# Kernel tuning notes

Measured on AMD Instinct MI355X. Metric: run time of the kernel, lower is better.

The kernel has to match this reference:

```python
import jax, jax.numpy as jnp
import numpy as np

D_MODEL, N_HEADS, D_C, D_FF, N_EXPERTS, TOP_K = 1024, 16, 128, 2048, 8, 2
HEAD_DIM = D_MODEL // N_HEADS
THETA = 10000.0
RMS_EPS = float(np.finfo(np.float32).eps)  # torch nn.RMSNorm default eps


def rmsnorm(x, w):
    var = jnp.mean(x * x, axis=-1, keepdims=True)
    return x * jax.lax.rsqrt(var + RMS_EPS) * w


def rotate_half(x):
    x1, x2 = jnp.split(x, 2, axis=-1)
    return jnp.concatenate([-x2, x1], axis=-1)


def rope_cos_sin(ts):
    # ts: (B, L) float timestamps -> cos, sin: (B, L, HEAD_DIM)
    freqs = 1.0 / THETA ** (jnp.arange(0, HEAD_DIM, 2, dtype=jnp.float32) / HEAD_DIM)
    t = ts[..., None] * freqs            # (B, L, HEAD_DIM//2)
    emb = jnp.concatenate([t, t], axis=-1)
    return jnp.cos(emb), jnp.sin(emb)


def setup_inputs() -> dict:
    key = jax.random.key(0)
    ks = jax.random.split(key, 16)
    B, L, D = 4, 1024, D_MODEL
    s = 0.02
    inp = {
        "x": jax.random.normal(ks[0], (B, L, D), jnp.float32),
        "timestamps_q": jnp.tile(jnp.arange(L, dtype=jnp.float32), (B, 1)),
        "timestamps_kv": jnp.tile(jnp.arange(L, dtype=jnp.float32), (B, 1)),
        "attn_norm_w": jnp.ones((D,), jnp.float32),
        "ffn_norm_w": jnp.ones((D,), jnp.float32),
        "w_kv_c": jax.random.normal(ks[1], (D_C, D), jnp.float32) * s,
        "w_kc_up": jax.random.normal(ks[2], (D, D_C), jnp.float32) * s,
        "w_vc_up": jax.random.normal(ks[3], (D, D_C), jnp.float32) * s,
        "w_qr": jax.random.normal(ks[4], (D, D), jnp.float32) * s,
        "w_kr": jax.random.normal(ks[5], (D, D), jnp.float32) * s,
        "w_o": jax.random.normal(ks[6], (D, D), jnp.float32) * s,
        "gate_w": jax.random.normal(ks[7], (N_EXPERTS, D), jnp.float32) * s,
        "expert_bias": jnp.zeros((N_EXPERTS,), jnp.float32),
        "w1": jax.random.normal(ks[8], (N_EXPERTS, 2 * D_FF, D), jnp.float32) * s,
        "w2": jax.random.normal(ks[9], (N_EXPERTS, D, 2 * D_FF), jnp.float32) * s,
    }
    return inp


def reference(x, timestamps_q, timestamps_kv, attn_norm_w, ffn_norm_w,
              w_kv_c, w_kc_up, w_vc_up, w_qr, w_kr, w_o,
              gate_w, expert_bias, w1, w2):
    B, L, D = x.shape
    H, hd = N_HEADS, HEAD_DIM
    scale = hd ** -0.5

    # ---- MLA attention (pre-norm) ----
    h = rmsnorm(x, attn_norm_w)
    c_kv = h @ w_kv_c.T                                    # (B,L,d_c)
    k_c = (c_kv @ w_kc_up.T).reshape(B, L, H, hd).transpose(0, 2, 1, 3)
    v_c = (c_kv @ w_vc_up.T).reshape(B, L, H, hd).transpose(0, 2, 1, 3)
    q_r = (h @ w_qr.T).reshape(B, L, H, hd).transpose(0, 2, 1, 3)
    k_r = (h @ w_kr.T).reshape(B, L, H, hd).transpose(0, 2, 1, 3)

    cos_q, _sin_q = rope_cos_sin(timestamps_q)
    cos_k, _sin_k = rope_cos_sin(timestamps_kv)
    cos_q = cos_q[:, None]  # (B,1,L,hd)
    cos_k = cos_k[:, None]
    # Faithful to source: apply_rotary_pos_emb(q, k, cos_q, cos_k) -> sin := cos_k
    q_r = q_r * cos_q + rotate_half(q_r) * cos_k
    k_r = k_r * cos_q + rotate_half(k_r) * cos_k

    qs = q_r * scale
    attn = jnp.einsum("bhqd,bhkd->bhqk", qs, k_c) + jnp.einsum("bhqd,bhkd->bhqk", qs, k_r)
    attn_w = jax.nn.softmax(attn, axis=-1)
    out = jnp.einsum("bhqk,bhkd->bhqd", attn_w, v_c)
    out = out.transpose(0, 2, 1, 3).reshape(B, L, D) @ w_o.T
    x1 = x + out

    # ---- MoE FFN (pre-norm) ----
    hn = rmsnorm(x1, ffn_norm_w).reshape(-1, D)            # (T, D)
    T = hn.shape[0]
    gate_logits = hn @ gate_w.T + expert_bias              # (T, E)
    gate_probs = jax.nn.softmax(gate_logits, axis=-1)
    topk_w, topk_i = jax.lax.top_k(gate_probs, TOP_K)
    topk_w = topk_w / jnp.sum(topk_w, axis=-1, keepdims=True)

    # dense (T, E) routing weights (top-k indices are unique per token)
    wd = jnp.zeros((T, N_EXPERTS), x.dtype).at[jnp.arange(T)[:, None], topk_i].add(topk_w)

    hmid = jax.nn.silu(jnp.einsum("td,ekd->tek", hn, w1))  # (T,E,2*d_ff)
    y = jnp.einsum("tek,edk->ted", hmid, w2)               # (T,E,D)
    moe_out = jnp.einsum("ted,te->td", y, wd).reshape(B, L, D)

    expert_counts = jnp.zeros((N_EXPERTS,), jnp.float32).at[topk_i.ravel()].add(1.0)
    return x1 + moe_out, expert_counts
```

## Files before the change

kernel.cpp:

```cpp
#include <hip/hip_runtime.h>
#include <hip/hip_bf16.h>

typedef __hip_bfloat16 bf16;
typedef __attribute__((ext_vector_type(8))) unsigned short ushort8v;
typedef __bf16 bf16x8 __attribute__((ext_vector_type(8)));
typedef float f32x4 __attribute__((ext_vector_type(4)));

#define NTOK 4096
#define DMODEL 1024
#define NHEADS 16
#define HD 64
#define DC 128
#define DFF2 4096
#define NEXP 8
#define LSEQ 1024
#define NBATCH 4
#define RMS_EPS 1.1920928955078125e-07f

union U8 { ushort8v u; bf16x8 b; };

__device__ __forceinline__ float bf2f(unsigned short u) {
  return __uint_as_float(((unsigned int)u) << 16);
}
__device__ __forceinline__ unsigned short f2bf(float f) {
  unsigned int u = __float_as_uint(f);
  unsigned int r = (u + 0x7FFF + ((u >> 16) & 1)) >> 16;
  return (unsigned short)r;
}
__device__ __forceinline__ void gload_lds16(const unsigned short* g, unsigned short* l) {
  __builtin_amdgcn_global_load_lds(
      (__attribute__((address_space(1))) void*)(const_cast<unsigned short*>(g)),
      (__attribute__((address_space(3))) void*)(l), 16, 0, 0);
}

__global__ __launch_bounds__(256)
void rmsnorm_kernel(const float* __restrict__ x, const float* __restrict__ w,
                    float* __restrict__ o, unsigned short* __restrict__ ob) {
  int t = blockIdx.x;
  int tid = threadIdx.x;
  const float4* xr = (const float4*)(x + (size_t)t * DMODEL);
  float4 v = xr[tid];
  float ss = v.x * v.x + v.y * v.y + v.z * v.z + v.w * v.w;
#pragma unroll
  for (int off = 32; off > 0; off >>= 1) ss += __shfl_xor(ss, off);
  __shared__ float red[4];
  int wid = tid >> 6, lane = tid & 63;
  if (lane == 0) red[wid] = ss;
  __syncthreads();
  float tot = red[0] + red[1] + red[2] + red[3];
  float scale = rsqrtf(tot * (1.0f / DMODEL) + RMS_EPS);
  float4 wv = ((const float4*)w)[tid];
  float4 ov;
  ov.x = v.x * scale * wv.x;
  ov.y = v.y * scale * wv.y;
  ov.z = v.z * scale * wv.z;
  ov.w = v.w * scale * wv.w;
  if (o) ((float4*)(o + (size_t)t * DMODEL))[tid] = ov;
  if (ob) {
    unsigned short* orow = ob + (size_t)t * DMODEL + tid * 4;
    orow[0] = f2bf(ov.x); orow[1] = f2bf(ov.y);
    orow[2] = f2bf(ov.z); orow[3] = f2bf(ov.w);
  }
}

__global__ __launch_bounds__(256)
void cvt_bf16_kernel(const float* __restrict__ in, unsigned short* __restrict__ o, int n8) {
  int stride = gridDim.x * 256;
  for (int i = blockIdx.x * 256 + threadIdx.x; i < n8; i += stride) {
    float4 a = ((const float4*)in)[2 * i];
    float4 b = ((const float4*)in)[2 * i + 1];
    ushort8v u;
    u[0] = f2bf(a.x); u[1] = f2bf(a.y); u[2] = f2bf(a.z); u[3] = f2bf(a.w);
    u[4] = f2bf(b.x); u[5] = f2bf(b.y); u[6] = f2bf(b.z); u[7] = f2bf(b.w);
    *(ushort8v*)(o + (size_t)i * 8) = u;
  }
}

__global__ __launch_bounds__(256)
void gemm_bf16(const unsigned short* __restrict__ Ab, const unsigned short* __restrict__ Wb,
               float* __restrict__ Cf, const float* __restrict__ addend, int N, int K) {
  __shared__ __align__(16) unsigned short As[128 * 64];
  __shared__ __align__(16) unsigned short Bs[128 * 64];
  int row0 = blockIdx.y * 128;
  int col0 = blockIdx.x * 128;
  int tid = threadIdx.x;
  int w = tid >> 6, l = tid & 63;
  int lr = l >> 3;
  int lc = (l & 7) * 8;

  const unsigned short* aSrc[4];
  const unsigned short* bSrc[4];
#pragma unroll
  for (int i = 0; i < 4; ++i) {
    aSrc[i] = Ab + (size_t)(row0 + i * 32 + w * 8 + lr) * K + lc;
    bSrc[i] = Wb + (size_t)(col0 + i * 32 + w * 8 + lr) * K + lc;
  }

  f32x4 acc[4][4] = {};
  int wr = w >> 1, wc = w & 1;
  int ln = l & 15, lq = l >> 4;

  for (int k0 = 0; k0 < K; k0 += 64) {
#pragma unroll
    for (int i = 0; i < 4; ++i) {
      gload_lds16(aSrc[i] + k0, &As[(i * 4 + w) * 512]);
      gload_lds16(bSrc[i] + k0, &Bs[(i * 4 + w) * 512]);
    }
    __syncthreads();
#pragma unroll
    for (int kk = 0; kk < 2; ++kk) {
      bf16x8 af[4], bfr[4];
#pragma unroll
      for (int m = 0; m < 4; ++m)
        af[m] = *(const bf16x8*)&As[(wr * 64 + m * 16 + ln) * 64 + kk * 32 + lq * 8];
#pragma unroll
      for (int n = 0; n < 4; ++n)
        bfr[n] = *(const bf16x8*)&Bs[(wc * 64 + n * 16 + ln) * 64 + kk * 32 + lq * 8];
#pragma unroll
      for (int m = 0; m < 4; ++m)
#pragma unroll
        for (int n = 0; n < 4; ++n)
          acc[m][n] = __builtin_amdgcn_mfma_f32_16x16x32_bf16(af[m], bfr[n], acc[m][n], 0, 0, 0);
    }
    __syncthreads();
  }

#pragma unroll
  for (int m = 0; m < 4; ++m) {
#pragma unroll
    for (int j = 0; j < 4; ++j) {
      int row = row0 + wr * 64 + m * 16 + lq * 4 + j;
      float* crow = Cf + (size_t)row * N + col0 + wc * 64 + ln;
      const float* arow = addend ? addend + (size_t)row * N + col0 + wc * 64 + ln : nullptr;
#pragma unroll
      for (int n = 0; n < 4; ++n) {
        float vv = acc[m][n][j];
        if (addend) vv += arow[n * 16];
        crow[n * 16] = vv;
      }
    }
  }
}

__global__ __launch_bounds__(256)
void gemm_proj(const unsigned short* __restrict__ Ab, const unsigned short* __restrict__ Wcat,
               float* __restrict__ d0, float* __restrict__ d1, float* __restrict__ d2,
               int c1, int c2, int s0, int s1, int s2, int K) {
  __shared__ __align__(16) unsigned short As[128 * 64];
  __shared__ __align__(16) unsigned short Bs[128 * 64];
  int row0 = blockIdx.y * 128;
  int col0 = blockIdx.x * 128;
  int tid = threadIdx.x;
  int w = tid >> 6, l = tid & 63;
  int lr = l >> 3;
  int lc = (l & 7) * 8;

  const unsigned short* aSrc[4];
  const unsigned short* bSrc[4];
#pragma unroll
  for (int i = 0; i < 4; ++i) {
    aSrc[i] = Ab + (size_t)(row0 + i * 32 + w * 8 + lr) * K + lc;
    bSrc[i] = Wcat + (size_t)(col0 + i * 32 + w * 8 + lr) * K + lc;
  }

  f32x4 acc[4][4] = {};
  int wr = w >> 1, wc = w & 1;
  int ln = l & 15, lq = l >> 4;

  for (int k0 = 0; k0 < K; k0 += 64) {
#pragma unroll
    for (int i = 0; i < 4; ++i) {
      gload_lds16(aSrc[i] + k0, &As[(i * 4 + w) * 512]);
      gload_lds16(bSrc[i] + k0, &Bs[(i * 4 + w) * 512]);
    }
    __syncthreads();
#pragma unroll
    for (int kk = 0; kk < 2; ++kk) {
      bf16x8 af[4], bfr[4];
#pragma unroll
      for (int m = 0; m < 4; ++m)
        af[m] = *(const bf16x8*)&As[(wr * 64 + m * 16 + ln) * 64 + kk * 32 + lq * 8];
#pragma unroll
      for (int n = 0; n < 4; ++n)
        bfr[n] = *(const bf16x8*)&Bs[(wc * 64 + n * 16 + ln) * 64 + kk * 32 + lq * 8];
#pragma unroll
      for (int m = 0; m < 4; ++m)
#pragma unroll
        for (int n = 0; n < 4; ++n)
          acc[m][n] = __builtin_amdgcn_mfma_f32_16x16x32_bf16(af[m], bfr[n], acc[m][n], 0, 0, 0);
    }
    __syncthreads();
  }

  float* dst;
  int cb, stride;
  if (col0 < c1) { dst = d0; cb = 0; stride = s0; }
  else if (col0 < c2) { dst = d1; cb = c1; stride = s1; }
  else { dst = d2; cb = c2; stride = s2; }
#pragma unroll
  for (int m = 0; m < 4; ++m) {
#pragma unroll
    for (int j = 0; j < 4; ++j) {
      int row = row0 + wr * 64 + m * 16 + lq * 4 + j;
      float* crow = dst + (size_t)row * stride + (col0 - cb) + wc * 64 + ln;
#pragma unroll
      for (int n = 0; n < 4; ++n) crow[n * 16] = acc[m][n][j];
    }
  }
}

template <int MODE>
__global__ __launch_bounds__(512, 2)
void moe_gemm256(const unsigned short* __restrict__ A, const unsigned short* __restrict__ W_,
                 unsigned short* __restrict__ Cb, const int* __restrict__ tok2e,
                 const int* __restrict__ ebase, const int* __restrict__ icnt) {
  constexpr int N = (MODE == 0) ? DFF2 : DMODEL;
  constexpr int K = (MODE == 0) ? DMODEL : DFF2;
  __shared__ __align__(16) unsigned short As[2][256 * 64];
  __shared__ __align__(16) unsigned short Bs[2][256 * 64];
  int e = blockIdx.z;
  int base = ebase[e];
  int cnt = icnt[e];
  int row0 = blockIdx.y * 256;
  if (row0 >= cnt) return;
  int col0 = blockIdx.x * 256;
  int tid = threadIdx.x;
  int w = tid >> 6, l = tid & 63;
  int lr = l >> 3, lc = (l & 7) * 8;

  const unsigned short* aP[4];
  const unsigned short* bP[4];
#pragma unroll
  for (int p = 0; p < 4; ++p) {
    int r = row0 + p * 64 + w * 8 + lr;
    r = r < cnt ? r : cnt - 1;
    if (MODE == 0)
      aP[p] = A + (size_t)(tok2e[base + r] >> 1) * K + lc;
    else
      aP[p] = A + (size_t)(base + r) * K + lc;
    bP[p] = W_ + (size_t)e * N * K + (size_t)(col0 + p * 64 + w * 8 + lr) * K + lc;
  }

  f32x4 acc[8][4] = {};
  int wm = w >> 2, wn = w & 3;
  int ln = l & 15, lq = l >> 4;

  constexpr int NT = K / 64;
#pragma unroll
  for (int p = 0; p < 4; ++p) {
    gload_lds16(aP[p], &As[0][(p * 64 + w * 8) * 64]);
    gload_lds16(bP[p], &Bs[0][(p * 64 + w * 8) * 64]);
  }
  __syncthreads();
  int cur = 0;
  for (int t = 0; t < NT; ++t) {
    if (t + 1 < NT) {
      int k0 = (t + 1) * 64;
#pragma unroll
      for (int p = 0; p < 4; ++p) {
        gload_lds16(aP[p] + k0, &As[cur ^ 1][(p * 64 + w * 8) * 64]);
        gload_lds16(bP[p] + k0, &Bs[cur ^ 1][(p * 64 + w * 8) * 64]);
      }
    }
    {
      const unsigned short* ab = &As[cur][0];
      const unsigned short* bb = &Bs[cur][0];
#pragma unroll
      for (int kk = 0; kk < 2; ++kk) {
        bf16x8 af[8], bfr[4];
#pragma unroll
        for (int m = 0; m < 8; ++m)
          af[m] = *(const bf16x8*)&ab[(wm * 128 + m * 16 + ln) * 64 + kk * 32 + lq * 8];
#pragma unroll
        for (int n = 0; n < 4; ++n)
          bfr[n] = *(const bf16x8*)&bb[(wn * 64 + n * 16 + ln) * 64 + kk * 32 + lq * 8];
#pragma unroll
        for (int m = 0; m < 8; ++m)
#pragma unroll
          for (int n = 0; n < 4; ++n)
            acc[m][n] = __builtin_amdgcn_mfma_f32_16x16x32_bf16(af[m], bfr[n], acc[m][n], 0, 0, 0);
      }
    }
    __syncthreads();
    cur ^= 1;
  }

#pragma unroll
  for (int m = 0; m < 8; ++m) {
#pragma unroll
    for (int j = 0; j < 4; ++j) {
      int r = row0 + wm * 128 + m * 16 + lq * 4 + j;
      if (r < cnt) {
        if (MODE == 0) {
          unsigned short* orow = Cb + (size_t)(base + r) * N + col0 + wn * 64 + ln;
#pragma unroll
          for (int n = 0; n < 4; ++n) {
            float v = acc[m][n][j];
            orow[n * 16] = f2bf(v / (1.f + __expf(-v)));
          }
        } else {
          int t2 = tok2e[base + r];
          unsigned short* orow = Cb + (size_t)t2 * N + col0 + wn * 64 + ln;
#pragma unroll
          for (int n = 0; n < 4; ++n) orow[n * 16] = f2bf(acc[m][n][j]);
        }
      }
    }
  }
}

__global__ __launch_bounds__(256)
void rope_kernel(float* __restrict__ q, float* __restrict__ k,
                 const float* __restrict__ kc, const float* __restrict__ tsq,
                 const float* __restrict__ tskv) {
  int t = blockIdx.x;
  int tid = threadIdx.x;
  __shared__ float cq[32], ck[32];
  if (tid < 32) {
    float fr = __expf(-(float)(2 * tid) * (1.0f / HD) * 9.210340371976184f);
    cq[tid] = cosf(tsq[t] * fr);
    ck[tid] = cosf(tskv[t] * fr);
  }
  __syncthreads();
  size_t rb = (size_t)t * DMODEL;
  for (int p = tid; p < 512; p += 256) {
    int hh = p >> 5, d = p & 31;
    int c1 = hh * 64 + d, c2 = c1 + 32;
    float cqd = cq[d], ckd = ck[d];
    float q1 = q[rb + c1], q2 = q[rb + c2];
    q[rb + c1] = (q1 * cqd - q2 * ckd) * 0.125f;
    q[rb + c2] = (q2 * cqd + q1 * ckd) * 0.125f;
    float k1 = k[rb + c1], k2 = k[rb + c2];
    k[rb + c1] = (k1 * cqd - k2 * ckd) + kc[rb + c1];
    k[rb + c2] = (k2 * cqd + k1 * ckd) + kc[rb + c2];
  }
}

__global__ __launch_bounds__(256)
void qk_split_kernel(const float* __restrict__ q, const float* __restrict__ k,
                     unsigned short* __restrict__ Qb, unsigned short* __restrict__ Kb) {
  int t = blockIdx.x;
  int b = t >> 10, lrow = t & 1023;
  int tid = threadIdx.x;
  int c = tid * 4;
  int hh = c >> 6, d = c & 63;
  size_t src = (size_t)t * DMODEL + c;
  size_t dst = ((size_t)(b * NHEADS + hh) * LSEQ + lrow) * HD + d;
  float4 qv = *(const float4*)(q + src);
  float4 kv = *(const float4*)(k + src);
  ushort4 u;
  u.x = f2bf(qv.x); u.y = f2bf(qv.y); u.z = f2bf(qv.z); u.w = f2bf(qv.w);
  *(ushort4*)(Qb + dst) = u;
  u.x = f2bf(kv.x); u.y = f2bf(kv.y); u.z = f2bf(kv.z); u.w = f2bf(kv.w);
  *(ushort4*)(Kb + dst) = u;
}

__global__ __launch_bounds__(256)
void v_split_kernel(const float* __restrict__ v, unsigned short* __restrict__ Vt) {
  __shared__ float tile[128][65];
  int bh = blockIdx.x;
  int lt = blockIdx.y;
  int b = bh >> 4, hh = bh & 15;
  int tid = threadIdx.x;
#pragma unroll
  for (int pass = 0; pass < 8; ++pass) {
    int r = pass * 16 + (tid >> 4);
    int dq = (tid & 15) * 4;
    float4 vv = *(const float4*)(v + (size_t)(b * 1024 + lt * 128 + r) * DMODEL + hh * 64 + dq);
    tile[r][dq + 0] = vv.x; tile[r][dq + 1] = vv.y;
    tile[r][dq + 2] = vv.z; tile[r][dq + 3] = vv.w;
  }
  __syncthreads();
  int d = tid >> 2, seg = (tid & 3) * 32;
  size_t obase = ((size_t)bh * HD + d) * LSEQ + lt * 128 + seg;
  for (int i = 0; i < 32; i += 4) {
    ushort4 u;
    u.x = f2bf(tile[seg + i][d]);
    u.y = f2bf(tile[seg + i + 1][d]);
    u.z = f2bf(tile[seg + i + 2][d]);
    u.w = f2bf(tile[seg + i + 3][d]);
    *(ushort4*)(Vt + obase + i) = u;
  }
}

__global__ __launch_bounds__(256, 2)
void attn_mfma(const unsigned short* __restrict__ Qb, const unsigned short* __restrict__ Kb,
               const unsigned short* __restrict__ Vt, unsigned short* __restrict__ ao) {
  __shared__ unsigned int plds[128 * 128];
  int bh = blockIdx.y;
  int qt = blockIdx.x;
  int tid = threadIdx.x;
  int w = tid >> 6, l = tid & 63;
  int ln = l & 15, lq = l >> 4;
  size_t kvbase = (size_t)bh * LSEQ * HD;
  int qrow0 = qt * 128 + w * 32;

  bf16x8 qh[2][2];
#pragma unroll
  for (int mi = 0; mi < 2; ++mi)
#pragma unroll
    for (int ks = 0; ks < 2; ++ks) {
      size_t o = kvbase + (size_t)(qrow0 + mi * 16 + ln) * HD + ks * 32 + lq * 8;
      qh[mi][ks] = *(const bf16x8*)(Qb + o);
    }

  float l_run[2][4] = {};
  f32x4 oacc[2][4] = {};

  for (int kt = 0; kt < 8; ++kt) {
    int k0 = kt * 128;
    f32x4 sacc[2][8] = {};
#pragma unroll
    for (int ni = 0; ni < 8; ++ni) {
      size_t ko = kvbase + (size_t)(k0 + ni * 16 + ln) * HD + lq * 8;
      bf16x8 kh0 = *(const bf16x8*)(Kb + ko);
      bf16x8 kh1 = *(const bf16x8*)(Kb + ko + 32);
#pragma unroll
      for (int mi = 0; mi < 2; ++mi) {
        f32x4 a = sacc[mi][ni];
        a = __builtin_amdgcn_mfma_f32_16x16x32_bf16(qh[mi][0], kh0, a, 0, 0, 0);
        a = __builtin_amdgcn_mfma_f32_16x16x32_bf16(qh[mi][1], kh1, a, 0, 0, 0);
        sacc[mi][ni] = a;
      }
    }
#pragma unroll
    for (int mi = 0; mi < 2; ++mi)
#pragma unroll
      for (int j = 0; j < 4; ++j) {
        float rs = 0.f;
#pragma unroll
        for (int ni = 0; ni < 8; ++ni) {
          float p = __expf(sacc[mi][ni][j]);
          sacc[mi][ni][j] = p;
          rs += p;
        }
        rs += __shfl_xor(rs, 1);
        rs += __shfl_xor(rs, 2);
        rs += __shfl_xor(rs, 4);
        rs += __shfl_xor(rs, 8);
        l_run[mi][j] += rs;
      }
#pragma unroll
    for (int mi = 0; mi < 2; ++mi)
#pragma unroll
      for (int ni = 0; ni < 8; ++ni)
#pragma unroll
        for (int j = 0; j < 4; ++j) {
          int row = w * 32 + mi * 16 + lq * 4 + j;
          int col = ni * 16 + ln;
          unsigned int u = ((unsigned int)f2bf(sacc[mi][ni][j])) << 16;
          plds[row * 128 + (col ^ ((row & 3) << 3))] = u;
        }
    __syncthreads();
#pragma unroll
    for (int ksp = 0; ksp < 4; ++ksp) {
      bf16x8 ph[2];
#pragma unroll
      for (int mi = 0; mi < 2; ++mi) {
        int row = w * 32 + mi * 16 + ln;
        int c0 = ksp * 32 + lq * 8;
        const unsigned int* pp = &plds[row * 128 + (c0 ^ ((row & 3) << 3))];
        uint4 u0 = *(const uint4*)pp;
        uint4 u1 = *(const uint4*)(pp + 4);
        unsigned int uu[8] = {u0.x, u0.y, u0.z, u0.w, u1.x, u1.y, u1.z, u1.w};
        U8 uh;
#pragma unroll
        for (int jj = 0; jj < 8; ++jj) uh.u[jj] = (unsigned short)(uu[jj] >> 16);
        ph[mi] = uh.b;
      }
#pragma unroll
      for (int ni = 0; ni < 4; ++ni) {
        size_t vo = kvbase + (size_t)(ni * 16 + ln) * LSEQ + k0 + ksp * 32 + lq * 8;
        bf16x8 vh = *(const bf16x8*)(Vt + vo);
#pragma unroll
        for (int mi = 0; mi < 2; ++mi)
          oacc[mi][ni] = __builtin_amdgcn_mfma_f32_16x16x32_bf16(ph[mi], vh, oacc[mi][ni], 0, 0, 0);
      }
    }
    __syncthreads();
  }

  int b = bh >> 4, hh = bh & 15;
#pragma unroll
  for (int mi = 0; mi < 2; ++mi) {
    float inv[4];
#pragma unroll
    for (int j = 0; j < 4; ++j) inv[j] = 1.0f / l_run[mi][j];
#pragma unroll
    for (int ni = 0; ni < 4; ++ni)
#pragma unroll
      for (int j = 0; j < 4; ++j) {
        int tok = b * 1024 + qt * 128 + w * 32 + mi * 16 + lq * 4 + j;
        int col = hh * 64 + ni * 16 + ln;
        ao[(size_t)tok * DMODEL + col] = f2bf(oacc[mi][ni][j] * inv[j]);
      }
  }
}

__global__ __launch_bounds__(256)
void gate_kernel(const float* __restrict__ hn, const float* __restrict__ gw,
                 const float* __restrict__ bias, int* __restrict__ ti,
                 float* __restrict__ tw, int* __restrict__ icnt,
                 float* __restrict__ counts_out) {
  int t = blockIdx.x * 4 + (threadIdx.x >> 6);
  int lane = threadIdx.x & 63;
  const float* hrow = hn + (size_t)t * DMODEL;
  float acc[NEXP];
#pragma unroll
  for (int e = 0; e < NEXP; ++e) acc[e] = 0.f;
  for (int d = lane; d < DMODEL; d += 64) {
    float hv = hrow[d];
#pragma unroll
    for (int e = 0; e < NEXP; ++e) acc[e] += hv * gw[e * DMODEL + d];
  }
#pragma unroll
  for (int e = 0; e < NEXP; ++e)
#pragma unroll
    for (int off = 32; off > 0; off >>= 1) acc[e] += __shfl_xor(acc[e], off);
  if (lane == 0) {
    float lg[NEXP], ex[NEXP];
    float mx = -1e30f;
#pragma unroll
    for (int e = 0; e < NEXP; ++e) {
      lg[e] = acc[e] + bias[e];
      mx = fmaxf(mx, lg[e]);
    }
#pragma unroll
    for (int e = 0; e < NEXP; ++e) ex[e] = expf(lg[e] - mx);
    int i0 = 0;
    float p0 = ex[0];
#pragma unroll
    for (int e = 1; e < NEXP; ++e)
      if (ex[e] > p0) { p0 = ex[e]; i0 = e; }
    int i1 = -1;
    float p1 = -1.f;
#pragma unroll
    for (int e = 0; e < NEXP; ++e)
      if (e != i0 && ex[e] > p1) { p1 = ex[e]; i1 = e; }
    float wsum = p0 + p1;
    ti[2 * t] = i0;
    ti[2 * t + 1] = i1;
    tw[2 * t] = p0 / wsum;
    tw[2 * t + 1] = p1 / wsum;
    atomicAdd(&icnt[i0], 1);
    atomicAdd(&icnt[i1], 1);
    atomicAdd(&counts_out[i0], 1.0f);
    atomicAdd(&counts_out[i1], 1.0f);
  }
}

__global__ void init_kernel(float* __restrict__ counts_out, int* __restrict__ icnt,
                            int* __restrict__ cursor) {
  int i = threadIdx.x;
  if (i < NEXP) {
    counts_out[i] = 0.f;
    icnt[i] = 0;
    cursor[i] = 0;
  }
}

__global__ void scan_kernel(const int* __restrict__ icnt, int* __restrict__ ebase) {
  if (threadIdx.x == 0) {
    int s = 0;
    for (int e = 0; e < NEXP; ++e) {
      ebase[e] = s;
      s += icnt[e];
    }
  }
}

__global__ __launch_bounds__(256)
void scatter_kernel(const int* __restrict__ ti, const int* __restrict__ ebase,
                    int* __restrict__ cursor, int* __restrict__ tok2e) {
  int t = blockIdx.x * 256 + threadIdx.x;
#pragma unroll
  for (int s = 0; s < 2; ++s) {
    int e = ti[2 * t + s];
    int pos = atomicAdd(&cursor[e], 1);
    tok2e[ebase[e] + pos] = 2 * t + s;
  }
}

__global__ __launch_bounds__(256)
void combine_kernel(const float* __restrict__ x1, const unsigned short* __restrict__ y,
                    const float* __restrict__ tw, float* __restrict__ out) {
  int idx = blockIdx.x * 256 + threadIdx.x;
  int t = idx >> 8, c = idx & 255;
  float w0 = tw[2 * t], w1 = tw[2 * t + 1];
  float4 a = ((const float4*)x1)[idx];
  const unsigned short* y0 = y + (size_t)(2 * t) * DMODEL + c * 4;
  const unsigned short* y1 = y0 + DMODEL;
  ushort4 u0 = *(const ushort4*)y0;
  ushort4 u1 = *(const ushort4*)y1;
  float4 o;
  o.x = a.x + w0 * bf2f(u0.x) + w1 * bf2f(u1.x);
  o.y = a.y + w0 * bf2f(u0.y) + w1 * bf2f(u1.y);
  o.z = a.z + w0 * bf2f(u0.z) + w1 * bf2f(u1.z);
  o.w = a.w + w0 * bf2f(u0.w) + w1 * bf2f(u1.w);
  ((float4*)out)[idx] = o;
}

extern "C" void kernel_launch(void* const* d_in, const int* in_sizes, int n_in,
                              void* d_out, int out_size, void* d_ws, size_t ws_size,
                              hipStream_t stream) {
  (void)in_sizes; (void)n_in; (void)ws_size;
  const float* x = (const float*)d_in[0];
  const float* tsq = (const float*)d_in[1];
  const float* tskv = (const float*)d_in[2];
  const float* attn_nw = (const float*)d_in[3];
  const float* ffn_nw = (const float*)d_in[4];
  const float* w_kv_c = (const float*)d_in[5];
  const float* w_kc_up = (const float*)d_in[6];
  const float* w_vc_up = (const float*)d_in[7];
  const float* w_qr = (const float*)d_in[8];
  const float* w_kr = (const float*)d_in[9];
  const float* w_o = (const float*)d_in[10];
  const float* gate_w = (const float*)d_in[11];
  const float* expert_bias = (const float*)d_in[12];
  const float* w1 = (const float*)d_in[13];
  const float* w2 = (const float*)d_in[14];

  float* out = (float*)d_out;
  float* counts_out = out + (out_size - NEXP);

  char* ws = (char*)d_ws;
  size_t off = 0;
  auto alloc = [&](size_t bytes) {
    char* p = ws + off;
    off += (bytes + 255) & ~(size_t)255;
    return p;
  };
  float* h   = (float*)alloc((size_t)NTOK * DMODEL * 4);
  float* qb  = (float*)alloc((size_t)NTOK * DMODEL * 4);
  float* kb  = (float*)alloc((size_t)NTOK * DMODEL * 4);
  float* vb  = (float*)alloc((size_t)NTOK * DMODEL * 4);
  float* kcb = (float*)alloc((size_t)NTOK * DMODEL * 4);
  float* ckv = (float*)alloc((size_t)NTOK * DC * 4);
  unsigned short* yb  = (unsigned short*)alloc((size_t)NTOK * 2 * DMODEL * 2);
  unsigned short* hb  = (unsigned short*)alloc((size_t)NTOK * DMODEL * 2);
  unsigned short* hmid = (unsigned short*)alloc((size_t)NTOK * 2 * DFF2 * 2);
  unsigned short* ckvb = (unsigned short*)alloc((size_t)NTOK * DC * 2);
  unsigned short* wbuf = (unsigned short*)alloc((size_t)2176 * DMODEL * 2);
  float* tw  = (float*)alloc((size_t)NTOK * 2 * 4);
  int* ti    = (int*)alloc((size_t)NTOK * 2 * 4);
  int* tok2e = (int*)alloc((size_t)NTOK * 2 * 4);
  int* icnt  = (int*)alloc(NEXP * 4);
  int* ebase = (int*)alloc(NEXP * 4);
  int* cursor = (int*)alloc(NEXP * 4);

  unsigned short* Qb = hmid;
  unsigned short* Kb = hmid + (size_t)4 * 1024 * 1024;
  unsigned short* Vt = hmid + (size_t)8 * 1024 * 1024;
  unsigned short* ao = hmid + (size_t)12 * 1024 * 1024;
  unsigned short* wxb = (unsigned short*)qb;

  init_kernel<<<1, 64, 0, stream>>>(counts_out, icnt, cursor);
  rmsnorm_kernel<<<NTOK, 256, 0, stream>>>(x, attn_nw, nullptr, hb);
  cvt_bf16_kernel<<<512, 256, 0, stream>>>(w_qr, wbuf, DMODEL * DMODEL / 8);
  cvt_bf16_kernel<<<512, 256, 0, stream>>>(w_kr, wbuf + (size_t)1024 * DMODEL, DMODEL * DMODEL / 8);
  cvt_bf16_kernel<<<64, 256, 0, stream>>>(w_kv_c, wbuf + (size_t)2048 * DMODEL, DC * DMODEL / 8);
  gemm_proj<<<dim3(17, 32), 256, 0, stream>>>(hb, wbuf, qb, kb, ckv,
                                              1024, 2048, DMODEL, DMODEL, DC, DMODEL);
  cvt_bf16_kernel<<<256, 256, 0, stream>>>(ckv, ckvb, NTOK * DC / 8);
  cvt_bf16_kernel<<<64, 256, 0, stream>>>(w_kc_up, wbuf, DMODEL * DC / 8);
  cvt_bf16_kernel<<<64, 256, 0, stream>>>(w_vc_up, wbuf + (size_t)1024 * DC, DMODEL * DC / 8);
  gemm_proj<<<dim3(16, 32), 256, 0, stream>>>(ckvb, wbuf, kcb, vb, vb,
                                              1024, 2048, DMODEL, DMODEL, DMODEL, DC);
  rope_kernel<<<NTOK, 256, 0, stream>>>(qb, kb, kcb, tsq, tskv);
  qk_split_kernel<<<NTOK, 256, 0, stream>>>(qb, kb, Qb, Kb);
  v_split_kernel<<<dim3(64, 8), 256, 0, stream>>>(vb, Vt);
  attn_mfma<<<dim3(8, 64), 256, 0, stream>>>(Qb, Kb, Vt, ao);
  cvt_bf16_kernel<<<512, 256, 0, stream>>>(w_o, wbuf, DMODEL * DMODEL / 8);
  gemm_bf16<<<dim3(8, 32), 256, 0, stream>>>(ao, wbuf, h, x, DMODEL, DMODEL);
  rmsnorm_kernel<<<NTOK, 256, 0, stream>>>(h, ffn_nw, qb, hb);
  gate_kernel<<<NTOK / 4, 256, 0, stream>>>(qb, gate_w, expert_bias, ti, tw, icnt, counts_out);
  scan_kernel<<<1, 64, 0, stream>>>(icnt, ebase);
  scatter_kernel<<<NTOK / 256, 256, 0, stream>>>(ti, ebase, cursor, tok2e);
  cvt_bf16_kernel<<<2048, 256, 0, stream>>>(w1, wxb, NEXP * DFF2 * DMODEL / 8);
  moe_gemm256<0><<<dim3(DFF2 / 256, NTOK / 256, NEXP), 512, 0, stream>>>(hb, wxb, hmid, tok2e, ebase, icnt);
  cvt_bf16_kernel<<<2048, 256, 0, stream>>>(w2, wxb, NEXP * DMODEL * DFF2 / 8);
  moe_gemm256<1><<<dim3(DMODEL / 256, NTOK / 256, NEXP), 512, 0, stream>>>(hmid, wxb, yb, tok2e, ebase, icnt);
  combine_kernel<<<NTOK, 256, 0, stream>>>(h, yb, tw, out);
}
```

Before: 814.0 us.

## Use three-stage pipelined MoE GEMM with 256x128 tiles and fuse RoPE with QK split

```diff
diff --git a/kernel.cpp b/kernel.cpp
--- a/kernel.cpp
+++ b/kernel.cpp
@@ -210,26 +210,27 @@
 }
 
 template <int MODE>
-__global__ __launch_bounds__(512, 2)
-void moe_gemm256(const unsigned short* __restrict__ A, const unsigned short* __restrict__ W_,
-                 unsigned short* __restrict__ Cb, const int* __restrict__ tok2e,
-                 const int* __restrict__ ebase, const int* __restrict__ icnt) {
+__global__ __launch_bounds__(512)
+void moe_pipe3(const unsigned short* __restrict__ A, const unsigned short* __restrict__ W_,
+               unsigned short* __restrict__ Cb, const int* __restrict__ tok2e,
+               const int* __restrict__ ebase, const int* __restrict__ icnt) {
   constexpr int N = (MODE == 0) ? DFF2 : DMODEL;
   constexpr int K = (MODE == 0) ? DMODEL : DFF2;
-  __shared__ __align__(16) unsigned short As[2][256 * 64];
-  __shared__ __align__(16) unsigned short Bs[2][256 * 64];
+  constexpr int NT = K / 64;
+  __shared__ __align__(16) unsigned short As[3][256 * 64];
+  __shared__ __align__(16) unsigned short Bs[3][128 * 64];
   int e = blockIdx.z;
   int base = ebase[e];
   int cnt = icnt[e];
   int row0 = blockIdx.y * 256;
   if (row0 >= cnt) return;
-  int col0 = blockIdx.x * 256;
+  int col0 = blockIdx.x * 128;
   int tid = threadIdx.x;
   int w = tid >> 6, l = tid & 63;
   int lr = l >> 3, lc = (l & 7) * 8;
 
   const unsigned short* aP[4];
-  const unsigned short* bP[4];
+  const unsigned short* bP[2];
 #pragma unroll
   for (int p = 0; p < 4; ++p) {
     int r = row0 + p * 64 + w * 8 + lr;
@@ -238,58 +239,62 @@
       aP[p] = A + (size_t)(tok2e[base + r] >> 1) * K + lc;
     else
       aP[p] = A + (size_t)(base + r) * K + lc;
-    bP[p] = W_ + (size_t)e * N * K + (size_t)(col0 + p * 64 + w * 8 + lr) * K + lc;
-  }
-
-  f32x4 acc[8][4] = {};
-  int wm = w >> 2, wn = w & 3;
+  }
+  const unsigned short* Wp = W_ + (size_t)e * N * K;
+#pragma unroll
+  for (int p = 0; p < 2; ++p)
+    bP[p] = Wp + (size_t)(col0 + p * 64 + w * 8 + lr) * K + lc;
+
+  auto STAGE = [&](int t, int s) {
+    int k0 = t * 64;
+#pragma unroll
+    for (int p = 0; p < 4; ++p) gload_lds16(aP[p] + k0, &As[s][(p * 64 + w * 8) * 64]);
+#pragma unroll
+    for (int p = 0; p < 2; ++p) gload_lds16(bP[p] + k0, &Bs[s][(p * 64 + w * 8) * 64]);
+  };
+
+  STAGE(0, 0);
+  STAGE(1, 1);
+  STAGE(2, 2);
+
+  f32x4 acc[4][4] = {};
+  int wm = w >> 1, wn = w & 1;
   int ln = l & 15, lq = l >> 4;
 
-  constexpr int NT = K / 64;
-#pragma unroll
-  for (int p = 0; p < 4; ++p) {
-    gload_lds16(aP[p], &As[0][(p * 64 + w * 8) * 64]);
-    gload_lds16(bP[p], &Bs[0][(p * 64 + w * 8) * 64]);
-  }
-  __syncthreads();
-  int cur = 0;
+  int s = 0;
   for (int t = 0; t < NT; ++t) {
-    if (t + 1 < NT) {
-      int k0 = (t + 1) * 64;
-#pragma unroll
-      for (int p = 0; p < 4; ++p) {
-        gload_lds16(aP[p] + k0, &As[cur ^ 1][(p * 64 + w * 8) * 64]);
-        gload_lds16(bP[p] + k0, &Bs[cur ^ 1][(p * 64 + w * 8) * 64]);
-      }
-    }
+    asm volatile("s_waitcnt vmcnt(12)" ::: "memory");
+    __builtin_amdgcn_s_barrier();
     {
-      const unsigned short* ab = &As[cur][0];
-      const unsigned short* bb = &Bs[cur][0];
+      const unsigned short* ab = &As[s][0];
+      const unsigned short* bb = &Bs[s][0];
 #pragma unroll
       for (int kk = 0; kk < 2; ++kk) {
-        bf16x8 af[8], bfr[4];
-#pragma unroll
-        for (int m = 0; m < 8; ++m)
-          af[m] = *(const bf16x8*)&ab[(wm * 128 + m * 16 + ln) * 64 + kk * 32 + lq * 8];
+        bf16x8 af[4], bfr[4];
+#pragma unroll
+        for (int m = 0; m < 4; ++m)
+          af[m] = *(const bf16x8*)&ab[(wm * 64 + m * 16 + ln) * 64 + kk * 32 + lq * 8];
 #pragma unroll
         for (int n = 0; n < 4; ++n)
           bfr[n] = *(const bf16x8*)&bb[(wn * 64 + n * 16 + ln) * 64 + kk * 32 + lq * 8];
 #pragma unroll
-        for (int m = 0; m < 8; ++m)
+        for (int m = 0; m < 4; ++m)
 #pragma unroll
           for (int n = 0; n < 4; ++n)
             acc[m][n] = __builtin_amdgcn_mfma_f32_16x16x32_bf16(af[m], bfr[n], acc[m][n], 0, 0, 0);
       }
     }
-    __syncthreads();
-    cur ^= 1;
-  }
-
-#pragma unroll
-  for (int m = 0; m < 8; ++m) {
+    asm volatile("s_waitcnt lgkmcnt(0)" ::: "memory");
+    __builtin_amdgcn_s_barrier();
+    if (t + 3 < NT) STAGE(t + 3, s);
+    s = (s == 2) ? 0 : s + 1;
+  }
+
+#pragma unroll
+  for (int m = 0; m < 4; ++m) {
 #pragma unroll
     for (int j = 0; j < 4; ++j) {
-      int r = row0 + wm * 128 + m * 16 + lq * 4 + j;
+      int r = row0 + wm * 64 + m * 16 + lq * 4 + j;
       if (r < cnt) {
         if (MODE == 0) {
           unsigned short* orow = Cb + (size_t)(base + r) * N + col0 + wn * 64 + ln;
@@ -310,9 +315,10 @@
 }
 
 __global__ __launch_bounds__(256)
-void rope_kernel(float* __restrict__ q, float* __restrict__ k,
-                 const float* __restrict__ kc, const float* __restrict__ tsq,
-                 const float* __restrict__ tskv) {
+void rope_qk_kernel(const float* __restrict__ q, const float* __restrict__ k,
+                    const float* __restrict__ kc, const float* __restrict__ tsq,
+                    const float* __restrict__ tskv,
+                    unsigned short* __restrict__ Qb, unsigned short* __restrict__ Kb) {
   int t = blockIdx.x;
   int tid = threadIdx.x;
   __shared__ float cq[32], ck[32];
@@ -322,37 +328,24 @@
     ck[tid] = cosf(tskv[t] * fr);
   }
   __syncthreads();
+  int b = t >> 10, lrow = t & 1023;
   size_t rb = (size_t)t * DMODEL;
   for (int p = tid; p < 512; p += 256) {
     int hh = p >> 5, d = p & 31;
     int c1 = hh * 64 + d, c2 = c1 + 32;
     float cqd = cq[d], ckd = ck[d];
     float q1 = q[rb + c1], q2 = q[rb + c2];
-    q[rb + c1] = (q1 * cqd - q2 * ckd) * 0.125f;
-    q[rb + c2] = (q2 * cqd + q1 * ckd) * 0.125f;
+    float rq1 = (q1 * cqd - q2 * ckd) * 0.125f;
+    float rq2 = (q2 * cqd + q1 * ckd) * 0.125f;
     float k1 = k[rb + c1], k2 = k[rb + c2];
-    k[rb + c1] = (k1 * cqd - k2 * ckd) + kc[rb + c1];
-    k[rb + c2] = (k2 * cqd + k1 * ckd) + kc[rb + c2];
-  }
-}
-
-__global__ __launch_bounds__(256)
-void qk_split_kernel(const float* __restrict__ q, const float* __restrict__ k,
-                     unsigned short* __restrict__ Qb, unsigned short* __restrict__ Kb) {
-  int t = blockIdx.x;
-  int b = t >> 10, lrow = t & 1023;
-  int tid = threadIdx.x;
-  int c = tid * 4;
-  int hh = c >> 6, d = c & 63;
-  size_t src = (size_t)t * DMODEL + c;
-  size_t dst = ((size_t)(b * NHEADS + hh) * LSEQ + lrow) * HD + d;
-  float4 qv = *(const float4*)(q + src);
-  float4 kv = *(const float4*)(k + src);
-  ushort4 u;
-  u.x = f2bf(qv.x); u.y = f2bf(qv.y); u.z = f2bf(qv.z); u.w = f2bf(qv.w);
-  *(ushort4*)(Qb + dst) = u;
-  u.x = f2bf(kv.x); u.y = f2bf(kv.y); u.z = f2bf(kv.z); u.w = f2bf(kv.w);
-  *(ushort4*)(Kb + dst) = u;
+    float rk1 = (k1 * cqd - k2 * ckd) + kc[rb + c1];
+    float rk2 = (k2 * cqd + k1 * ckd) + kc[rb + c2];
+    size_t dst = ((size_t)(b * NHEADS + hh) * LSEQ + lrow) * HD;
+    Qb[dst + d] = f2bf(rq1);
+    Qb[dst + d + 32] = f2bf(rq2);
+    Kb[dst + d] = f2bf(rk1);
+    Kb[dst + d + 32] = f2bf(rk2);
+  }
 }
 
 __global__ __launch_bounds__(256)
@@ -666,8 +659,7 @@
   cvt_bf16_kernel<<<64, 256, 0, stream>>>(w_vc_up, wbuf + (size_t)1024 * DC, DMODEL * DC / 8);
   gemm_proj<<<dim3(16, 32), 256, 0, stream>>>(ckvb, wbuf, kcb, vb, vb,
                                               1024, 2048, DMODEL, DMODEL, DMODEL, DC);
-  rope_kernel<<<NTOK, 256, 0, stream>>>(qb, kb, kcb, tsq, tskv);
-  qk_split_kernel<<<NTOK, 256, 0, stream>>>(qb, kb, Qb, Kb);
+  rope_qk_kernel<<<NTOK, 256, 0, stream>>>(qb, kb, kcb, tsq, tskv, Qb, Kb);
   v_split_kernel<<<dim3(64, 8), 256, 0, stream>>>(vb, Vt);
   attn_mfma<<<dim3(8, 64), 256, 0, stream>>>(Qb, Kb, Vt, ao);
   cvt_bf16_kernel<<<512, 256, 0, stream>>>(w_o, wbuf, DMODEL * DMODEL / 8);
@@ -677,8 +669,8 @@
   scan_kernel<<<1, 64, 0, stream>>>(icnt, ebase);
   scatter_kernel<<<NTOK / 256, 256, 0, stream>>>(ti, ebase, cursor, tok2e);
   cvt_bf16_kernel<<<2048, 256, 0, stream>>>(w1, wxb, NEXP * DFF2 * DMODEL / 8);
-  moe_gemm256<0><<<dim3(DFF2 / 256, NTOK / 256, NEXP), 512, 0, stream>>>(hb, wxb, hmid, tok2e, ebase, icnt);
+  moe_pipe3<0><<<dim3(DFF2 / 128, NTOK / 256, NEXP), 512, 0, stream>>>(hb, wxb, hmid, tok2e, ebase, icnt);
   cvt_bf16_kernel<<<2048, 256, 0, stream>>>(w2, wxb, NEXP * DMODEL * DFF2 / 8);
-  moe_gemm256<1><<<dim3(DMODEL / 256, NTOK / 256, NEXP), 512, 0, stream>>>(hmid, wxb, yb, tok2e, ebase, icnt);
+  moe_pipe3<1><<<dim3(DMODEL / 128, NTOK / 256, NEXP), 512, 0, stream>>>(hmid, wxb, yb, tok2e, ebase, icnt);
   combine_kernel<<<NTOK, 256, 0, stream>>>(h, yb, tw, out);
 }
```

Result: no change. 829.8 us (+1.9%).
